# Kernel tuning notes

Hardware: AMD Instinct MI355X
Metric: run time of the kernel (lower is better)

Reference implementation:

```python
import jax, jax.numpy as jnp
import numpy as np

B = 262144
EDGES_SRC = np.array([0, 0, 0, 0])
EDGES_DST = np.array([1, 2, 3, 4])
PRED_IDS = np.array([[0, 10, 14], [1, 11, 18], [2, 12, 22], [3, 13, 26]])
O_IDS = np.array([0, 1, 2, 3, 10, 11, 12, 13, 14, 18, 22, 26])


def _xavier(k, shape):
    fan_out, fan_in = shape
    bound = float(np.sqrt(6.0 / (fan_in + fan_out)))
    return jax.random.uniform(k, shape, jnp.float32, -bound, bound)


def setup_inputs() -> dict:
    key = jax.random.key(0)
    ks = jax.random.split(key, 12)
    return {
        "initial_c": jax.random.uniform(ks[0], (B, 30), jnp.float32),
        "initial_s": jax.random.normal(ks[1], (B, 9), jnp.float32),
        "current_c": jax.random.uniform(ks[2], (B, 30), jnp.float32),
        "eps": jax.random.normal(ks[3], (B, 8), jnp.float32),
        # GnnMessagePassing params (torch Linear: y = x @ W.T + b)
        "W1": _xavier(ks[4], (128, 13)), "b1": jnp.zeros(128, jnp.float32),
        "W2": _xavier(ks[5], (39, 128)), "b2": jnp.zeros(39, jnp.float32),
        "W3": _xavier(ks[6], (128, 39)), "b3": jnp.zeros(128, jnp.float32),
        "Wm": _xavier(ks[7], (8, 128)), "bm": jnp.zeros(8, jnp.float32),
        "Wv": _xavier(ks[8], (8, 128)), "bv": jnp.zeros(8, jnp.float32),
        # Decoder params: [25 -> 32 -> 12], sigmoid output (binary=True)
        "Wd1": _xavier(ks[9], (32, 25)), "bd1": jnp.zeros(32, jnp.float32),
        "Wd2": _xavier(ks[10], (12, 32)), "bd2": jnp.zeros(12, jnp.float32),
    }


def reference(initial_c, initial_s, current_c, eps,
              W1, b1, W2, b2, W3, b3, Wm, bm, Wv, bv, Wd1, bd1, Wd2, bd2):
    bsz = current_c.shape[0]
    eye = jnp.eye(5, dtype=current_c.dtype)
    # per-edge constant one-hot pair features: [4, 10]
    edge_onehot = jnp.concatenate([eye[EDGES_SRC], eye[EDGES_DST]], axis=-1)
    edge_onehot = jnp.broadcast_to(edge_onehot[:, None, :], (4, bsz, 10))
    # gather predicate triplets per edge: [B, 4, 3] -> [4, B, 3]
    preds = jnp.transpose(current_c[:, PRED_IDS], (1, 0, 2))
    inp_mp = jnp.concatenate([edge_onehot, preds], axis=-1)  # [4, B, 13]

    # message MLP + sum over edge dim
    x = jax.nn.relu(jnp.einsum('ebi,oi->ebo', inp_mp, W1) + b1)  # [4, B, 128]
    x = jax.nn.relu(jnp.einsum('ebi,oi->ebo', x, W2) + b2)       # [4, B, 39]
    x = x.sum(axis=0)                                            # [B, 39]
    x = jax.nn.relu(x @ W3.T + b3)                               # [B, 128]
    means = x @ Wm.T + bm                                        # [B, 8]
    log_var = x @ Wv.T + bv                                      # [B, 8]

    # reparameterization
    z = eps * jnp.exp(0.5 * log_var) + means

    # decoder: [one-hot(node 0) | initial_c[o_ids] | z] -> sigmoid MLP
    node0 = jnp.broadcast_to(eye[0], (bsz, 5))
    inp_dec = jnp.concatenate([node0, initial_c[:, O_IDS], z], axis=1)  # [B, 25]
    h = jax.nn.relu(inp_dec @ Wd1.T + bd1)
    recon_x = jax.nn.sigmoid(h @ Wd2.T + bd2)  # [B, 12]
    return recon_x, means, log_var, z
```

## Files before the change

### kernel.cpp

```cpp
#include <hip/hip_runtime.h>
#include <hip/hip_bf16.h>

#define TPB 256
#define PREP_BLOCKS 64

typedef __attribute__((ext_vector_type(8))) short short8;
typedef __attribute__((ext_vector_type(4))) float f32x4;

#define G_W2F   0
#define G_MVF   12288
#define G_D1F   16384
#define G_D2F   18432
#define G_CEAB  19456
#define G_B2P   23552
#define G_B3    23744
#define G_BMV   24256
#define G_D1C   24320
#define G_BD2   24448
#define G_W3F   24512
#define G_END   40896

__device__ __forceinline__ unsigned short f2bf(float f) {
    unsigned int u = __float_as_uint(f);
    unsigned int r = u + 0x7fffu + ((u >> 16) & 1u);
    return (unsigned short)(r >> 16);
}
__device__ __forceinline__ unsigned int pk(float a, float b) {
    __hip_bfloat162 h = __float22bfloat162_rn(make_float2(a, b));
    unsigned int u; __builtin_memcpy(&u, &h, 4); return u;
}

__global__ void prep_kernel(
    const float* __restrict__ W1, const float* __restrict__ b1,
    const float* __restrict__ W2, const float* __restrict__ b2,
    const float* __restrict__ W3, const float* __restrict__ b3,
    const float* __restrict__ Wm, const float* __restrict__ bm,
    const float* __restrict__ Wv, const float* __restrict__ bv,
    const float* __restrict__ Wd1, const float* __restrict__ bd1,
    const float* __restrict__ Wd2, const float* __restrict__ bd2,
    unsigned char* __restrict__ ws)
{
    const int g0 = blockIdx.x * TPB + threadIdx.x;
    const int gs = gridDim.x * TPB;
    unsigned short* w2f = (unsigned short*)(ws + G_W2F);
    for (int i = g0; i < 6144; i += gs) {
        int j = i & 7, lane = (i >> 3) & 63, ts = i >> 9;
        int t = ts >> 2, s = ts & 3, q = lane >> 4;
        int n = 16 * t + (lane & 15);
        int phys = 16 * (2 * s + (j >> 2)) + 4 * q + (j & 3);
        w2f[i] = (n < 39) ? f2bf(W2[n * 128 + phys]) : 0;
    }
    unsigned short* w3f = (unsigned short*)(ws + G_W3F);
    for (int i = g0; i < 8192; i += gs) {
        int j = i & 7, lane = (i >> 3) & 63, ns = i >> 9;
        int nt = ns >> 1, s = ns & 1, q = lane >> 4;
        int n = 16 * nt + (lane & 15);
        int phys = 16 * (2 * s + (j >> 2)) + 4 * q + (j & 3);
        w3f[i] = (phys < 39) ? f2bf(W3[n * 39 + phys]) : 0;
    }
    unsigned short* mvf = (unsigned short*)(ws + G_MVF);
    for (int i = g0; i < 2048; i += gs) {
        int j = i & 7, lane = (i >> 3) & 63, s = i >> 9;
        int q = lane >> 4, n = lane & 15;
        int phys = 16 * (2 * s + (j >> 2)) + 4 * q + (j & 3);
        mvf[i] = f2bf(n < 8 ? Wm[n * 128 + phys] : Wv[(n - 8) * 128 + phys]);
    }
    unsigned short* d1f = (unsigned short*)(ws + G_D1F);
    for (int i = g0; i < 1024; i += gs) {
        int j = i & 7, lane = (i >> 3) & 63, tt = i >> 9;
        int q = lane >> 4, n = 16 * tt + (lane & 15);
        int phys = 16 * (j >> 2) + 4 * q + (j & 3);
        d1f[i] = (phys < 20) ? f2bf(Wd1[n * 25 + 5 + phys]) : 0;
    }
    unsigned short* d2f = (unsigned short*)(ws + G_D2F);
    for (int i = g0; i < 512; i += gs) {
        int j = i & 7, lane = i >> 3;
        int q = lane >> 4, n = lane & 15;
        int phys = 16 * (j >> 2) + 4 * q + (j & 3);
        d2f[i] = (n < 12) ? f2bf(Wd2[n * 32 + phys]) : 0;
    }
    unsigned short* ceab = (unsigned short*)(ws + G_CEAB);
    for (int i = g0; i < 2048; i += gs) {
        int c = i & 3, n = (i >> 2) & 127, e = i >> 9;
        float v = (c < 3) ? W1[n * 13 + 10 + c]
                          : (W1[n * 13 + 0] + W1[n * 13 + 6 + e] + b1[n]);
        ceab[i] = f2bf(v);
    }
    float* fb = (float*)(ws + G_B2P);
    for (int i = g0; i < 48; i += gs) fb[i] = (i < 39) ? b2[i] : 0.f;
    fb = (float*)(ws + G_B3);
    for (int i = g0; i < 128; i += gs) fb[i] = b3[i];
    fb = (float*)(ws + G_BMV);
    for (int i = g0; i < 16; i += gs) fb[i] = (i < 8) ? bm[i] : bv[i - 8];
    fb = (float*)(ws + G_D1C);
    for (int i = g0; i < 32; i += gs) fb[i] = Wd1[i * 25 + 0] + bd1[i];
    fb = (float*)(ws + G_BD2);
    for (int i = g0; i < 16; i += gs) fb[i] = (i < 12) ? bd2[i] : 0.f;
}

union S8 { short8 v; uint4 u; };

#define MFMA(a, b, c) __builtin_amdgcn_mfma_f32_16x16x32_bf16(a, b, c, 0, 0, 0)

__global__ __launch_bounds__(TPB, 2) void vae_mfma(
    const float* __restrict__ ic, const float* __restrict__ cc,
    const float* __restrict__ eps,
    const unsigned char* __restrict__ ws,
    float* __restrict__ out, int B)
{
    __shared__ __attribute__((aligned(16))) unsigned char lds[G_END];
    const int tid = threadIdx.x;

    {
        const uint4* src = (const uint4*)ws;
        uint4* dst = (uint4*)lds;
        #pragma unroll
        for (int it = 0; it < 10; it++) {
            int idx = it * TPB + tid;
            if (idx < G_END / 16) dst[idx] = src[idx];
        }
    }
    __syncthreads();

    const int lane = tid & 63, w = tid >> 6;
    const int quad = lane >> 4, n16 = lane & 15;
    const bool q0 = (quad == 0);
    const long rb = ((long)blockIdx.x * 4 + w) * 16;
    const long Rl = rb + n16;

    unsigned int bpx[4] = {0,0,0,0}, bpy[4] = {0,0,0,0};
    if (q0) {
        const float* crow = cc + Rl * 30;
        float2 u0 = *(const float2*)(crow);
        float2 u1 = *(const float2*)(crow + 2);
        float2 u2 = *(const float2*)(crow + 10);
        float2 u3 = *(const float2*)(crow + 12);
        bpx[0] = pk(u0.x, u2.x); bpy[0] = pk(crow[14], 1.0f);
        bpx[1] = pk(u0.y, u2.y); bpy[1] = pk(crow[18], 1.0f);
        bpx[2] = pk(u1.x, u3.x); bpy[2] = pk(crow[22], 1.0f);
        bpx[3] = pk(u1.y, u3.y); bpy[3] = pk(crow[26], 1.0f);
    }

    S8 W2F[12];
    #pragma unroll
    for (int ts = 0; ts < 12; ts++)
        W2F[ts].u = *(const uint4*)(lds + G_W2F + (ts * 64 + lane) * 16);
    const float* b2p = (const float*)(lds + G_B2P);
    f32x4 b2q[3];
    #pragma unroll
    for (int t = 0; t < 3; t++)
        b2q[t] = *(const f32x4*)(b2p + 16 * t + 4 * quad);

    f32x4 ss0 = {0,0,0,0}, ss1 = {0,0,0,0}, ss2 = {0,0,0,0};

    #pragma unroll
    for (int e = 0; e < 4; e++) {
        S8 bp;
        bp.u.x = bpx[e]; bp.u.y = bpy[e]; bp.u.z = 0u; bp.u.w = 0u;
        const unsigned long long* cb =
            (const unsigned long long*)(lds + G_CEAB + e * 1024);
        S8 xf[4];
        #pragma unroll
        for (int mt = 0; mt < 8; mt++) {
            unsigned long long bw = cb[mt * 16 + n16];
            S8 af;
            af.u.x = q0 ? (unsigned int)bw : 0u;
            af.u.y = q0 ? (unsigned int)(bw >> 32) : 0u;
            af.u.z = 0u; af.u.w = 0u;
            f32x4 z4 = {0,0,0,0};
            f32x4 cr = MFMA(af.v, bp.v, z4);
            unsigned int lo = pk(fmaxf(cr[0], 0.f), fmaxf(cr[1], 0.f));
            unsigned int hi = pk(fmaxf(cr[2], 0.f), fmaxf(cr[3], 0.f));
            if ((mt & 1) == 0) { xf[mt >> 1].u.x = lo; xf[mt >> 1].u.y = hi; }
            else               { xf[mt >> 1].u.z = lo; xf[mt >> 1].u.w = hi; }
        }
        f32x4 c0 = b2q[0], c1 = b2q[1], c2 = b2q[2];
        #pragma unroll
        for (int s = 0; s < 4; s++) {
            c0 = MFMA(W2F[s].v,     xf[s].v, c0);
            c1 = MFMA(W2F[4 + s].v, xf[s].v, c1);
            c2 = MFMA(W2F[8 + s].v, xf[s].v, c2);
        }
        #pragma unroll
        for (int r = 0; r < 4; r++) {
            ss0[r] += fmaxf(c0[r], 0.f);
            ss1[r] += fmaxf(c1[r], 0.f);
            ss2[r] += fmaxf(c2[r], 0.f);
        }
    }

    S8 sf0, sf1;
    sf0.u.x = pk(ss0[0], ss0[1]); sf0.u.y = pk(ss0[2], ss0[3]);
    sf0.u.z = pk(ss1[0], ss1[1]); sf0.u.w = pk(ss1[2], ss1[3]);
    sf1.u.x = pk(ss2[0], ss2[1]); sf1.u.y = pk(ss2[2], ss2[3]);
    sf1.u.z = 0u; sf1.u.w = 0u;

    const uint4* w3l = (const uint4*)(lds + G_W3F);
    const float* b3p = (const float*)(lds + G_B3);
    S8 hf[4];
    #pragma unroll
    for (int nt = 0; nt < 8; nt++) {
        f32x4 c = *(const f32x4*)(b3p + nt * 16 + 4 * quad);
        S8 a0, a1;
        a0.u = w3l[(nt * 2 + 0) * 64 + lane];
        a1.u = w3l[(nt * 2 + 1) * 64 + lane];
        c = MFMA(a0.v, sf0.v, c);
        c = MFMA(a1.v, sf1.v, c);
        unsigned int lo = pk(fmaxf(c[0], 0.f), fmaxf(c[1], 0.f));
        unsigned int hi = pk(fmaxf(c[2], 0.f), fmaxf(c[3], 0.f));
        if ((nt & 1) == 0) { hf[nt >> 1].u.x = lo; hf[nt >> 1].u.y = hi; }
        else               { hf[nt >> 1].u.z = lo; hf[nt >> 1].u.w = hi; }
    }

    f32x4 cm = *(const f32x4*)((const float*)(lds + G_BMV) + 4 * quad);
    #pragma unroll
    for (int s = 0; s < 4; s++) {
        S8 a; a.u = *(const uint4*)(lds + G_MVF + (s * 64 + lane) * 16);
        cm = MFMA(a.v, hf[s].v, cm);
    }

    const int addrLv = ((lane + 32) & 63) << 2;
    float lvv[4];
    #pragma unroll
    for (int r = 0; r < 4; r++)
        lvv[r] = __int_as_float(
            __builtin_amdgcn_ds_bpermute(addrLv, __float_as_int(cm[r])));
    float4 ev = *(const float4*)(eps + Rl * 8 + 4 * (quad & 1));
    f32x4 zz;
    zz[0] = fmaf(ev.x, __expf(0.5f * lvv[0]), cm[0]);
    zz[1] = fmaf(ev.y, __expf(0.5f * lvv[1]), cm[1]);
    zz[2] = fmaf(ev.z, __expf(0.5f * lvv[2]), cm[2]);
    zz[3] = fmaf(ev.w, __expf(0.5f * lvv[3]), cm[3]);
    float* pml = (float*)((quad < 2) ? (out + (long)B * 12) : (out + (long)B * 20));
    *(float4*)(pml + Rl * 8 + 4 * (quad & 1)) = *(float4*)&cm;
    if (quad < 2)
        *(float4*)(out + (long)B * 28 + Rl * 8 + 4 * quad) = *(float4*)&zz;

    const int addrZ = (n16 + (q0 ? 16 : 0)) << 2;
    float zr[4];
    #pragma unroll
    for (int r = 0; r < 4; r++)
        zr[r] = __int_as_float(
            __builtin_amdgcn_ds_bpermute(addrZ, __float_as_int(zz[r])));

    const float* irow = ic + Rl * 30;
    float d0, d1, d2, d3;
    if (quad == 3)      { d0 = zr[0];    d1 = zr[1];    d2 = zr[2];    d3 = zr[3]; }
    else if (quad == 2) { d0 = irow[14]; d1 = irow[18]; d2 = irow[22]; d3 = irow[26]; }
    else {
        const float* p = irow + (quad ? 10 : 0);
        float2 u0 = *(const float2*)(p);
        float2 u1 = *(const float2*)(p + 2);
        d0 = u0.x; d1 = u0.y; d2 = u1.x; d3 = u1.y;
    }
    S8 df;
    df.u.x = pk(d0, d1);
    df.u.y = pk(d2, d3);
    df.u.z = q0 ? pk(zr[0], zr[1]) : 0u;
    df.u.w = q0 ? pk(zr[2], zr[3]) : 0u;

    const float* d1c = (const float*)(lds + G_D1C);
    S8 a;
    f32x4 ct = *(const f32x4*)(d1c + 4 * quad);
    a.u = *(const uint4*)(lds + G_D1F + (0 * 64 + lane) * 16);
    f32x4 h0 = MFMA(a.v, df.v, ct);
    ct = *(const f32x4*)(d1c + 16 + 4 * quad);
    a.u = *(const uint4*)(lds + G_D1F + (1 * 64 + lane) * 16);
    f32x4 h1 = MFMA(a.v, df.v, ct);
    S8 hf2;
    hf2.u.x = pk(fmaxf(h0[0], 0.f), fmaxf(h0[1], 0.f));
    hf2.u.y = pk(fmaxf(h0[2], 0.f), fmaxf(h0[3], 0.f));
    hf2.u.z = pk(fmaxf(h1[0], 0.f), fmaxf(h1[1], 0.f));
    hf2.u.w = pk(fmaxf(h1[2], 0.f), fmaxf(h1[3], 0.f));

    f32x4 c2 = *(const f32x4*)((const float*)(lds + G_BD2) + 4 * quad);
    S8 a2; a2.u = *(const uint4*)(lds + G_D2F + lane * 16);
    c2 = MFMA(a2.v, hf2.v, c2);
    if (quad < 3) {
        float4 o;
        o.x = 1.f / (1.f + __expf(-c2[0]));
        o.y = 1.f / (1.f + __expf(-c2[1]));
        o.z = 1.f / (1.f + __expf(-c2[2]));
        o.w = 1.f / (1.f + __expf(-c2[3]));
        *(float4*)(out + Rl * 12 + 4 * quad) = o;
    }
}

extern "C" void kernel_launch(void* const* d_in, const int* in_sizes, int n_in,
                              void* d_out, int out_size, void* d_ws, size_t ws_size,
                              hipStream_t stream) {
    const float* ic  = (const float*)d_in[0];
    const float* cc  = (const float*)d_in[2];
    const float* eps = (const float*)d_in[3];

    const int B = in_sizes[3] / 8;
    const int nblocks = B / 64;

    prep_kernel<<<PREP_BLOCKS, TPB, 0, stream>>>(
        (const float*)d_in[4],  (const float*)d_in[5],
        (const float*)d_in[6],  (const float*)d_in[7],
        (const float*)d_in[8],  (const float*)d_in[9],
        (const float*)d_in[10], (const float*)d_in[11],
        (const float*)d_in[12], (const float*)d_in[13],
        (const float*)d_in[14], (const float*)d_in[15],
        (const float*)d_in[16], (const float*)d_in[17],
        (unsigned char*)d_ws);
    vae_mfma<<<nblocks, TPB, 0, stream>>>(
        ic, cc, eps, (const unsigned char*)d_ws, (float*)d_out, B);
}
```

Measured before the change: 181.8 us.

## Redistribute MFMA K-operands across quads to remove cross-lane permutes

```diff
diff --git a/kernel.cpp b/kernel.cpp
--- a/kernel.cpp
+++ b/kernel.cpp
@@ -28,6 +28,9 @@
 __device__ __forceinline__ unsigned int pk(float a, float b) {
     __hip_bfloat162 h = __float22bfloat162_rn(make_float2(a, b));
     unsigned int u; __builtin_memcpy(&u, &h, 4); return u;
+}
+__device__ __forceinline__ unsigned short bfbits(float v) {
+    return (unsigned short)(pk(v, v) & 0xffffu);
 }
 
 __global__ void prep_kernel(
@@ -69,8 +72,10 @@
     for (int i = g0; i < 1024; i += gs) {
         int j = i & 7, lane = (i >> 3) & 63, tt = i >> 9;
         int q = lane >> 4, n = 16 * tt + (lane & 15);
-        int phys = 16 * (j >> 2) + 4 * q + (j & 3);
-        d1f[i] = (phys < 20) ? f2bf(Wd1[n * 25 + 5 + phys]) : 0;
+        float v = 0.f;
+        if (q == 0)      v = Wd1[n * 25 + 5 + j];
+        else if (j < 4)  v = Wd1[n * 25 + 13 + 4 * (q - 1) + j];
+        d1f[i] = (q == 0 || j < 4) ? f2bf(v) : 0;
     }
     unsigned short* d2f = (unsigned short*)(ws + G_D2F);
     for (int i = g0; i < 512; i += gs) {
@@ -81,9 +86,12 @@
     }
     unsigned short* ceab = (unsigned short*)(ws + G_CEAB);
     for (int i = g0; i < 2048; i += gs) {
-        int c = i & 3, n = (i >> 2) & 127, e = i >> 9;
-        float v = (c < 3) ? W1[n * 13 + 10 + c]
-                          : (W1[n * 13 + 0] + W1[n * 13 + 6 + e] + b1[n]);
+        int lane = i & 63, mt = (i >> 6) & 7, e = i >> 9;
+        int q = lane >> 4, n = 16 * mt + (lane & 15);
+        float v = (q == 0) ? W1[n * 13 + 10]
+                : (q == 1) ? W1[n * 13 + 11]
+                : (q == 2) ? W1[n * 13 + 12]
+                           : (W1[n * 13 + 0] + W1[n * 13 + 6 + e] + b1[n]);
         ceab[i] = f2bf(v);
     }
     float* fb = (float*)(ws + G_B2P);
@@ -124,21 +132,30 @@
 
     const int lane = tid & 63, w = tid >> 6;
     const int quad = lane >> 4, n16 = lane & 15;
-    const bool q0 = (quad == 0);
     const long rb = ((long)blockIdx.x * 4 + w) * 16;
     const long Rl = rb + n16;
 
-    unsigned int bpx[4] = {0,0,0,0}, bpy[4] = {0,0,0,0};
-    if (q0) {
+    unsigned int bpv[4];
+    {
         const float* crow = cc + Rl * 30;
-        float2 u0 = *(const float2*)(crow);
-        float2 u1 = *(const float2*)(crow + 2);
-        float2 u2 = *(const float2*)(crow + 10);
-        float2 u3 = *(const float2*)(crow + 12);
-        bpx[0] = pk(u0.x, u2.x); bpy[0] = pk(crow[14], 1.0f);
-        bpx[1] = pk(u0.y, u2.y); bpy[1] = pk(crow[18], 1.0f);
-        bpx[2] = pk(u1.x, u3.x); bpy[2] = pk(crow[22], 1.0f);
-        bpx[3] = pk(u1.y, u3.y); bpy[3] = pk(crow[26], 1.0f);
+        float pv0, pv1, pv2, pv3;
+        if (quad == 0) {
+            float2 t0 = *(const float2*)(crow);
+            float2 t1 = *(const float2*)(crow + 2);
+            pv0 = t0.x; pv1 = t0.y; pv2 = t1.x; pv3 = t1.y;
+        } else if (quad == 1) {
+            float2 t0 = *(const float2*)(crow + 10);
+            float2 t1 = *(const float2*)(crow + 12);
+            pv0 = t0.x; pv1 = t0.y; pv2 = t1.x; pv3 = t1.y;
+        } else if (quad == 2) {
+            pv0 = crow[14]; pv1 = crow[18]; pv2 = crow[22]; pv3 = crow[26];
+        } else {
+            pv0 = pv1 = pv2 = pv3 = 1.0f;
+        }
+        bpv[0] = (unsigned int)bfbits(pv0);
+        bpv[1] = (unsigned int)bfbits(pv1);
+        bpv[2] = (unsigned int)bfbits(pv2);
+        bpv[3] = (unsigned int)bfbits(pv3);
     }
 
     S8 W2F[12];
@@ -156,17 +173,15 @@
     #pragma unroll
     for (int e = 0; e < 4; e++) {
         S8 bp;
-        bp.u.x = bpx[e]; bp.u.y = bpy[e]; bp.u.z = 0u; bp.u.w = 0u;
-        const unsigned long long* cb =
-            (const unsigned long long*)(lds + G_CEAB + e * 1024);
+        bp.u.x = bpv[e]; bp.u.y = 0u; bp.u.z = 0u; bp.u.w = 0u;
+        const unsigned short* cb2 =
+            (const unsigned short*)(lds + G_CEAB + e * 1024);
         S8 xf[4];
         #pragma unroll
         for (int mt = 0; mt < 8; mt++) {
-            unsigned long long bw = cb[mt * 16 + n16];
             S8 af;
-            af.u.x = q0 ? (unsigned int)bw : 0u;
-            af.u.y = q0 ? (unsigned int)(bw >> 32) : 0u;
-            af.u.z = 0u; af.u.w = 0u;
+            af.u.x = (unsigned int)cb2[mt * 64 + lane];
+            af.u.y = 0u; af.u.z = 0u; af.u.w = 0u;
             f32x4 z4 = {0,0,0,0};
             f32x4 cr = MFMA(af.v, bp.v, z4);
             unsigned int lo = pk(fmaxf(cr[0], 0.f), fmaxf(cr[1], 0.f));
@@ -212,52 +227,55 @@
         else               { hf[nt >> 1].u.z = lo; hf[nt >> 1].u.w = hi; }
     }
 
-    f32x4 cm = *(const f32x4*)((const float*)(lds + G_BMV) + 4 * quad);
+    f32x4 cm  = *(const f32x4*)((const float*)(lds + G_BMV) + 4 * quad);
+    f32x4 cm2 = *(const f32x4*)((const float*)(lds + G_BMV) + 4 * ((quad + 2) & 3));
+    const int laneSw = quad * 16 + ((n16 + 8) & 15);
     #pragma unroll
     for (int s = 0; s < 4; s++) {
-        S8 a; a.u = *(const uint4*)(lds + G_MVF + (s * 64 + lane) * 16);
-        cm = MFMA(a.v, hf[s].v, cm);
-    }
-
-    const int addrLv = ((lane + 32) & 63) << 2;
-    float lvv[4];
-    #pragma unroll
-    for (int r = 0; r < 4; r++)
-        lvv[r] = __int_as_float(
-            __builtin_amdgcn_ds_bpermute(addrLv, __float_as_int(cm[r])));
+        S8 a, a2;
+        a.u  = *(const uint4*)(lds + G_MVF + (s * 64 + lane) * 16);
+        a2.u = *(const uint4*)(lds + G_MVF + (s * 64 + laneSw) * 16);
+        cm  = MFMA(a.v,  hf[s].v, cm);
+        cm2 = MFMA(a2.v, hf[s].v, cm2);
+    }
+
     float4 ev = *(const float4*)(eps + Rl * 8 + 4 * (quad & 1));
     f32x4 zz;
-    zz[0] = fmaf(ev.x, __expf(0.5f * lvv[0]), cm[0]);
-    zz[1] = fmaf(ev.y, __expf(0.5f * lvv[1]), cm[1]);
-    zz[2] = fmaf(ev.z, __expf(0.5f * lvv[2]), cm[2]);
-    zz[3] = fmaf(ev.w, __expf(0.5f * lvv[3]), cm[3]);
+    {
+        const bool lo2 = (quad < 2);
+        float mn0 = lo2 ? cm[0] : cm2[0], lv0 = lo2 ? cm2[0] : cm[0];
+        float mn1 = lo2 ? cm[1] : cm2[1], lv1 = lo2 ? cm2[1] : cm[1];
+        float mn2 = lo2 ? cm[2] : cm2[2], lv2 = lo2 ? cm2[2] : cm[2];
+        float mn3 = lo2 ? cm[3] : cm2[3], lv3 = lo2 ? cm2[3] : cm[3];
+        zz[0] = fmaf(ev.x, __expf(0.5f * lv0), mn0);
+        zz[1] = fmaf(ev.y, __expf(0.5f * lv1), mn1);
+        zz[2] = fmaf(ev.z, __expf(0.5f * lv2), mn2);
+        zz[3] = fmaf(ev.w, __expf(0.5f * lv3), mn3);
+    }
     float* pml = (float*)((quad < 2) ? (out + (long)B * 12) : (out + (long)B * 20));
     *(float4*)(pml + Rl * 8 + 4 * (quad & 1)) = *(float4*)&cm;
     if (quad < 2)
         *(float4*)(out + (long)B * 28 + Rl * 8 + 4 * quad) = *(float4*)&zz;
 
-    const int addrZ = (n16 + (q0 ? 16 : 0)) << 2;
-    float zr[4];
-    #pragma unroll
-    for (int r = 0; r < 4; r++)
-        zr[r] = __int_as_float(
-            __builtin_amdgcn_ds_bpermute(addrZ, __float_as_int(zz[r])));
-
-    const float* irow = ic + Rl * 30;
-    float d0, d1, d2, d3;
-    if (quad == 3)      { d0 = zr[0];    d1 = zr[1];    d2 = zr[2];    d3 = zr[3]; }
-    else if (quad == 2) { d0 = irow[14]; d1 = irow[18]; d2 = irow[22]; d3 = irow[26]; }
-    else {
-        const float* p = irow + (quad ? 10 : 0);
-        float2 u0 = *(const float2*)(p);
-        float2 u1 = *(const float2*)(p + 2);
-        d0 = u0.x; d1 = u0.y; d2 = u1.x; d3 = u1.y;
-    }
     S8 df;
-    df.u.x = pk(d0, d1);
-    df.u.y = pk(d2, d3);
-    df.u.z = q0 ? pk(zr[0], zr[1]) : 0u;
-    df.u.w = q0 ? pk(zr[2], zr[3]) : 0u;
+    if (quad == 0) {
+        const float* irow = ic + Rl * 30;
+        float2 a0 = *(const float2*)(irow);
+        float2 a1 = *(const float2*)(irow + 2);
+        float2 a2 = *(const float2*)(irow + 10);
+        float2 a3 = *(const float2*)(irow + 12);
+        df.u.x = pk(a0.x, a0.y); df.u.y = pk(a1.x, a1.y);
+        df.u.z = pk(a2.x, a2.y); df.u.w = pk(a3.x, a3.y);
+    } else if (quad == 1) {
+        const float* irow = ic + Rl * 30;
+        df.u.x = pk(irow[14], irow[18]);
+        df.u.y = pk(irow[22], irow[26]);
+        df.u.z = 0u; df.u.w = 0u;
+    } else {
+        df.u.x = pk(zz[0], zz[1]);
+        df.u.y = pk(zz[2], zz[3]);
+        df.u.z = 0u; df.u.w = 0u;
+    }
 
     const float* d1c = (const float*)(lds + G_D1C);
     S8 a;
```

Result: no change. 181.8 us (+0.0%).
